# Performance work log

Measured on AMD Instinct MI355X. Metric: run time of the kernel, lower is better.

The kernel has to match this reference:

```python
import jax, jax.numpy as jnp
import numpy as np

P, N, M, B = 5, 30000, 50000, 256
T, C, L, ED, H, EMB, TD, NL = 13, 16, 3, 4, 128, 64, 5, 3
SRC = jnp.repeat(jnp.arange(P), P)  # edge type i = src*P + dst
DST = jnp.tile(jnp.arange(P), P)


def _affine(x, W, b):
    # x: [P, n, i], W: [P, i, o], b: [P, o]
    return jnp.einsum('pni,pio->pno', x, W) + b[:, None, :]


def _lrelu(x, s=0.01):
    return jnp.where(x >= 0, x, s * x)


def _gat(h, W, a_s, a_d, We, a_e, b, edge_index, edge_attr):
    # h: [P, N, H]; per-edge-type GATConv (heads=1, no self loops) then hetero 'max' aggregation
    hs, hd = h[SRC], h[DST]                       # [25, N, H]
    xl = jnp.einsum('enh,ehf->enf', hs, W)        # transformed source features
    xr = jnp.einsum('enh,ehf->enf', hd, W)
    als = jnp.einsum('enf,ef->en', xl, a_s)
    ald = jnp.einsum('enf,ef->en', xr, a_d)

    def per_type(xl_e, als_e, ald_e, ea, We_e, ae_e, ei):
        src, dst = ei[0], ei[1]
        alpha = als_e[src] + ald_e[dst] + (ea @ We_e) @ ae_e
        alpha = jnp.where(alpha >= 0, alpha, 0.2 * alpha)  # GAT negative_slope=0.2
        amax = jax.ops.segment_max(alpha, dst, num_segments=N)
        ex = jnp.exp(alpha - amax[dst])
        den = jax.ops.segment_sum(ex, dst, num_segments=N)
        w = ex / (den[dst] + 1e-16)
        return jax.ops.segment_sum(w[:, None] * xl_e[src], dst, num_segments=N)

    out = jax.vmap(per_type)(xl, als, ald, edge_attr, We, a_e, edge_index)
    out = out + b[:, None, :]
    return out.reshape(P, P, N, H).max(axis=0)  # HeteroConv aggr='max' over source types


def setup_inputs():
    key = jax.random.key(0)
    ks = iter(jax.random.split(key, 64))
    def nrm(shape, s=1.0):
        return jax.random.normal(next(ks), shape, dtype=jnp.float32) * s
    w = 0.05
    inp = {
        'x': nrm((P, N, T)),
        'cond_x': nrm((P, N, C + L)),
        'edge_attr': nrm((P * P, M, ED)),
        'timesteps': jax.random.uniform(next(ks), (B,), dtype=jnp.float32),
        'te1_W': nrm((1, TD), w), 'te1_b': nrm((TD,), w),
        'te2_W': nrm((TD, TD), w), 'te2_b': nrm((TD,), w),
        'emb_W': nrm((P, T + L, EMB), w), 'emb_b': nrm((P, EMB), w),
        'cemb_W': nrm((P, C, EMB), w), 'cemb_b': nrm((P, EMB), w),
        'pa_W': nrm((P, 2 * EMB, 2 * EMB), w), 'pa_b': nrm((P, 2 * EMB), w),
        'pc_W': nrm((P, 2 * EMB, EMB), w), 'pc_b': nrm((P, EMB), w),
        'sl0_W': nrm((P, EMB + TD, H), w), 'sl0_b': nrm((P, H), w),
        'sl12_W': nrm((2, P, H + TD, H), w), 'sl12_b': nrm((2, P, H), w),
        'slout_W': nrm((P, H + TD, T), w), 'slout_b': nrm((P, T), w),
        'gat_W': nrm((NL, P * P, H, H), w), 'gat_as': nrm((NL, P * P, H), w),
        'gat_ad': nrm((NL, P * P, H), w), 'gat_We': nrm((NL, P * P, ED, H), w),
        'gat_ae': nrm((NL, P * P, H), w), 'gat_b': nrm((NL, P * P, H), w),
        'xc_W': nrm((NL, P, H, H // 2), w), 'xc_b': nrm((NL, P, H // 2), w),
        'cc_W': nrm((NL, P, H, H // 2), w), 'cc_b': nrm((NL, P, H // 2), w),
        'ca_W': nrm((NL, P, H, H), w), 'ca_b': nrm((NL, P, H), w),
        'batch_idx': jax.random.randint(next(ks), (P, N), 0, B),
        'edge_index': jax.random.randint(next(ks), (P * P, 2, M), 0, N),
    }
    return inp


def reference(x, cond_x, edge_attr, timesteps, te1_W, te1_b, te2_W, te2_b,
              emb_W, emb_b, cemb_W, cemb_b, pa_W, pa_b, pc_W, pc_b,
              sl0_W, sl0_b, sl12_W, sl12_b, slout_W, slout_b,
              gat_W, gat_as, gat_ad, gat_We, gat_ae, gat_b,
              xc_W, xc_b, cc_W, cc_b, ca_W, ca_b, batch_idx, edge_index):
    # time embedding: Linear(1,TD) -> SiLU -> Linear(TD,TD)
    temb = jax.nn.silu(timesteps[:, None] @ te1_W + te1_b) @ te2_W + te2_b  # [B, TD]
    cond, latent = cond_x[..., :C], cond_x[..., C:]
    h = _affine(jnp.concatenate([x, latent], -1), emb_W, emb_b)            # [P,N,EMB]
    ce = _affine(cond, cemb_W, cemb_b)
    h = jnp.concatenate([h, ce], -1)                                       # [P,N,2EMB]
    h = jax.nn.sigmoid(_affine(h, pa_W, pa_b)) * h                         # attention pooling
    h = _affine(h, pc_W, pc_b)                                             # [P,N,EMB]
    nt = temb[batch_idx]                                                   # [P,N,TD]
    h = jnp.concatenate([h, nt], -1)
    for l in range(NL):
        if l > 0:
            h = jnp.concatenate([h, nt], -1)
        Wl, bl = (sl0_W, sl0_b) if l == 0 else (sl12_W[l - 1], sl12_b[l - 1])
        h = _lrelu(_affine(h, Wl, bl))                                     # [P,N,H]
        comm = _lrelu(_gat(h, gat_W[l], gat_as[l], gat_ad[l], gat_We[l], gat_ae[l], gat_b[l], edge_index, edge_attr))
        h = jnp.concatenate([_affine(h, xc_W[l], xc_b[l]), _affine(comm, cc_W[l], cc_b[l])], -1)
        h = h + jax.nn.sigmoid(_affine(h, ca_W[l], ca_b[l])) * h
    h = jnp.concatenate([h, nt], -1)
    return _affine(h, slout_W, slout_b)                                    # [P,N,T]
```

## Files before the change

kernel.cpp:

```cpp
#include <hip/hip_runtime.h>
#include <cstdio>

using bf8 = __attribute__((ext_vector_type(8))) short;
using f4v = __attribute__((ext_vector_type(4))) float;
typedef unsigned short u16;
typedef unsigned int u32;

#define DEV __device__ __forceinline__

DEV float bf2f(u16 u){ return __uint_as_float(((u32)u) << 16); }
DEV u16 f2bf(float f){ u32 u = __float_as_uint(f); return (u16)((u + 0x7fffu + ((u >> 16) & 1u)) >> 16); }
DEV float sigm(float v){ return 1.f / (1.f + __expf(-v)); }

constexpr int P5 = 5, NN = 30000, MM = 50000, NE = 25, BB = 256;
constexpr int KC = 96;
constexpr int RS = KC * 2 + 16;
constexpr int RSA = 272;

__global__ void temb_k(const float* ts, const float* w1, const float* b1,
                       const float* w2, const float* b2, float* temb){
  int i = blockIdx.x * blockDim.x + threadIdx.x;
  if (i >= BB) return;
  float t = ts[i]; float z[5];
#pragma unroll
  for (int j = 0; j < 5; ++j){ float u = t * w1[j] + b1[j]; z[j] = u * sigm(u); }
#pragma unroll
  for (int j2 = 0; j2 < 5; ++j2){
    float s = b2[j2];
#pragma unroll
    for (int j = 0; j < 5; ++j) s += z[j] * w2[j * 5 + j2];
    temb[i * 5 + j2] = s;
  }
}

__global__ void wtransE_k(const float* __restrict__ W, u16* __restrict__ Wt,
                          int Kreal, int Kpad, int Nreal, int Nalloc, int total){
  int idx = blockIdx.x * blockDim.x + threadIdx.x;
  if (idx >= total) return;
  int k = idx % Kpad;
  int t2 = idx / Kpad;
  int f = t2 % Nalloc;
  int b = t2 / Nalloc;
  float v = (k < Kreal && f < Nreal) ? W[((size_t)b * Kreal + k) * Nreal + f] : 0.f;
  Wt[idx] = f2bf(v);
}

__global__ void embw_k(const float* emb_W, const float* emb_b, const float* cemb_W, const float* cemb_b,
                       u16* Wc, float* bc){
  int b = blockIdx.x, f = threadIdx.x;
  for (int k = 0; k < 32; ++k){
    float v = 0.f;
    if (f < 64){ if (k < 16) v = emb_W[((size_t)b * 16 + k) * 64 + f]; }
    else       { if (k >= 16) v = cemb_W[((size_t)b * 16 + (k - 16)) * 64 + (f - 64)]; }
    Wc[((size_t)b * 128 + f) * 32 + k] = f2bf(v);
  }
  bc[b * 128 + f] = (f < 64) ? emb_b[b * 64 + f] : cemb_b[b * 64 + (f - 64)];
}

__global__ void gwtT_k(const float* __restrict__ gW, u16* __restrict__ gWt){
  int idx = blockIdx.x * blockDim.x + threadIdx.x;
  if (idx >= 75 * 128 * 128) return;
  int h = idx & 127, f = (idx >> 7) & 127, le = idx >> 14;
  gWt[idx] = f2bf(gW[(size_t)le * 16384 + h * 128 + f]);
}

__global__ void gatred_k(const float* gW, const float* gas, const float* gad,
                         const float* gWe, const float* gae,
                         float* wswd, float* eaw){
  int le = blockIdx.x; int h = threadIdx.x;
  const float* W = gW + (size_t)le * 16384;
  const float* as_ = gas + le * 128;
  const float* ad_ = gad + le * 128;
  float wsv = 0.f, wdv = 0.f;
  for (int f = 0; f < 128; ++f){
    float w = W[h * 128 + f];
    wsv += w * as_[f]; wdv += w * ad_[f];
  }
  wswd[le * 256 + h] = wsv;
  wswd[le * 256 + 128 + h] = wdv;
  if (h < 4){
    const float* We = gWe + (size_t)le * 512;
    const float* ae = gae + le * 128;
    float s = 0.f;
    for (int f = 0; f < 128; ++f) s += We[h * 128 + f] * ae[f];
    eaw[le * 4 + h] = s;
  }
}

__global__ void abuild_k(const float* x, const float* cx, u16* A0){
  int idx = blockIdx.x * blockDim.x + threadIdx.x;
  if (idx >= P5 * NN) return;
  const float* xr = x + (size_t)idx * 13;
  const float* cr = cx + (size_t)idx * 19;
  u16* a0 = A0 + (size_t)idx * 32;
#pragma unroll
  for (int i = 0; i < 13; ++i) a0[i] = f2bf(xr[i]);
#pragma unroll
  for (int i = 0; i < 3; ++i) a0[13 + i] = f2bf(cr[16 + i]);
#pragma unroll
  for (int i = 0; i < 16; ++i) a0[16 + i] = f2bf(cr[i]);
}

__global__ void ntfill_k(u16* buf, int pitch, int co, const int* bidx, const float* temb){
  int idx = blockIdx.x * blockDim.x + threadIdx.x;
  if (idx >= P5 * NN) return;
  int b = bidx[idx];
  u16* r = buf + (size_t)idx * pitch;
#pragma unroll
  for (int j = 0; j < 5; ++j) r[co + j] = f2bf(temb[b * 5 + j]);
  for (int j = co + 5; j < pitch; ++j) r[j] = 0;
}

__global__ void csr_count_k(const int* EI, int* cnt){
  int idx = blockIdx.x * blockDim.x + threadIdx.x;
  if (idx >= NE * MM) return;
  int e = idx / MM, m = idx % MM;
  int dst = EI[(size_t)e * 2 * MM + MM + m];
  atomicAdd(&cnt[e * NN + dst], 1);
}

__global__ __launch_bounds__(1024) void csr_scan_k(const int* cnt, int* off){
  int e = blockIdx.x, tid = threadIdx.x;
  int lane = tid & 63, wv = tid >> 6;
  __shared__ int wsum[16];
  int running = 0;
  for (int c = 0; c < 30; ++c){
    int idx = c * 1024 + tid;
    int v = (idx < NN) ? cnt[e * NN + idx] : 0;
    int s = v;
#pragma unroll
    for (int o = 1; o < 64; o <<= 1){
      int t = __shfl_up(s, o, 64);
      if (lane >= o) s += t;
    }
    if (lane == 63) wsum[wv] = s;
    __syncthreads();
    if (wv == 0 && lane < 16){
      int t = wsum[lane];
#pragma unroll
      for (int o = 1; o < 16; o <<= 1){
        int u = __shfl_up(t, o, 64);
        if (lane >= o) t += u;
      }
      wsum[lane] = t;
    }
    __syncthreads();
    int base = running + ((wv > 0) ? wsum[wv - 1] : 0);
    if (idx < NN) off[(size_t)e * (NN + 1) + idx] = base + s - v;
    running += wsum[15];
    __syncthreads();
  }
  if (tid == 0) off[(size_t)e * (NN + 1) + NN] = running;
}

__global__ void csr_fill_k(const int* EI, const int* off, int* cnt, int* mpos, int* srcC){
  int idx = blockIdx.x * blockDim.x + threadIdx.x;
  if (idx >= NE * MM) return;
  int e = idx / MM, m = idx % MM;
  int dst = EI[(size_t)e * 2 * MM + MM + m];
  int pos = off[(size_t)e * (NN + 1) + dst] + atomicAdd(&cnt[e * NN + dst], 1);
  mpos[idx] = pos;
  srcC[(size_t)e * MM + pos] = EI[(size_t)e * 2 * MM + m];
}

__global__ void eadot_k(const float* __restrict__ ea, const float* __restrict__ eaw,
                        const int* __restrict__ mpos, float* __restrict__ eadot){
  int idx = blockIdx.x * blockDim.x + threadIdx.x;
  if (idx >= 3 * NE * MM) return;
  int l = idx / (NE * MM);
  int rem = idx - l * NE * MM;
  int e = rem / MM, m = rem - e * MM;
  const float* a4 = ea + ((size_t)e * MM + m) * 4;
  const float* ew = eaw + (size_t)(l * NE + e) * 4;
  float d = a4[0] * ew[0] + a4[1] * ew[1] + a4[2] * ew[2] + a4[3] * ew[3];
  eadot[(size_t)l * NE * MM + (size_t)e * MM + mpos[rem]] = d;
}

__global__ __launch_bounds__(256) void dots2_k(const u16* __restrict__ hS, const float* __restrict__ wswd_l,
                                               float* __restrict__ als, float* __restrict__ ald){
  __shared__ u32 hl[64][65];
  __shared__ float wsl[10][129];
  int p = blockIdx.y;
  int n0 = blockIdx.x * 64;
  int tid = threadIdx.x;
  for (int i = tid; i < 10 * 128; i += 256){
    int col = i >> 7, k = i & 127;
    int e = (col < 5) ? (p * 5 + col) : ((col - 5) * 5 + p);
    wsl[col][k] = wswd_l[e * 256 + ((col < 5) ? 0 : 128) + k];
  }
  for (int i = tid; i < 64 * 64; i += 256){
    int r = i >> 6, kp = i & 63;
    int n = n0 + r;
    hl[r][kp] = (n < NN) ? ((const u32*)hS)[((size_t)p * NN + n) * 64 + kp] : 0u;
  }
  __syncthreads();
  int col = tid & 15, rbase = tid >> 4;
  if (col < 10){
#pragma unroll
    for (int pass = 0; pass < 4; ++pass){
      int r = rbase + pass * 16;
      int n = n0 + r;
      if (n >= NN) continue;
      float s = 0.f;
#pragma unroll
      for (int kp = 0; kp < 64; ++kp){
        u32 pr = hl[r][kp];
        s += bf2f((u16)(pr & 0xffffu)) * wsl[col][2 * kp]
           + bf2f((u16)(pr >> 16)) * wsl[col][2 * kp + 1];
      }
      if (col < 5) als[(size_t)(p * 5 + col) * NN + n] = s;
      else         ald[(size_t)((col - 5) * 5 + p) * NN + n] = s;
    }
  }
}

__global__ __launch_bounds__(256) void aexp_k(const float* __restrict__ als, const float* __restrict__ ald,
                                              const float* __restrict__ eadot_l, const int* __restrict__ srcC,
                                              const int* __restrict__ off, uint2* __restrict__ prec){
  int idx = blockIdx.x * blockDim.x + threadIdx.x;
  if (idx >= NE * NN) return;
  int e = idx / NN;
  int ro = off[(size_t)e + idx], re = off[(size_t)e + idx + 1];
  if (ro >= re) return;
  float av = ald[idx];
  const int* sc = srcC + (size_t)e * MM;
  const float* ed = eadot_l + (size_t)e * MM;
  const float* ale = als + (size_t)e * NN;
  float mx = -3.0e38f;
  for (int j = ro; j < re; ++j){
    float a = ale[sc[j]] + av + ed[j];
    a = (a >= 0.f) ? a : 0.2f * a;
    mx = fmaxf(mx, a);
  }
  for (int j = ro; j < re; ++j){
    int src = sc[j];
    float a = ale[src] + av + ed[j];
    a = (a >= 0.f) ? a : 0.2f * a;
    uint2 pr; pr.x = (u32)src; pr.y = __float_as_uint(__expf(a - mx));
    prec[(size_t)e * MM + j] = pr;
  }
}

__global__ __launch_bounds__(256) void agg3_k(const u16* __restrict__ hS, const uint2* __restrict__ prec,
                                              const int* __restrict__ off, u16* __restrict__ agghB,
                                              int pd0, int npd){
  int l = threadIdx.x & 63, w = threadIdx.x >> 6;
  int n0 = blockIdx.x * 8 + w;
  int n1 = n0 + 4;
  int y = blockIdx.y;
  int ps = y / npd, e = ps * 5 + pd0 + (y - ps * npd);
  const uint2* pe = prec + (size_t)e * MM;
  const int* offe = off + (size_t)e * (NN + 1);
  const u32* hb = (const u32*)hS + (size_t)ps * NN * 64 + l;
  int ro0 = 0, ln0 = 0, ro1 = 0, ln1 = 0;
  if (n0 < NN){ ro0 = offe[n0]; ln0 = offe[n0 + 1] - ro0; }
  if (n1 < NN){ ro1 = offe[n1]; ln1 = offe[n1 + 1] - ro1; }
  float den0 = 0.f, a00 = 0.f, a01 = 0.f;
  float den1 = 0.f, a10 = 0.f, a11 = 0.f;
  int mx = (ln0 > ln1) ? ln0 : ln1;
  for (int t = 0; t < mx; ++t){
    if (t < ln0){
      uint2 pr = pe[ro0 + t];
      float ex = __uint_as_float(pr.y);
      u32 hv = hb[(size_t)pr.x * 64];
      den0 += ex; a00 += ex * bf2f((u16)(hv & 0xffffu)); a01 += ex * bf2f((u16)(hv >> 16));
    }
    if (t < ln1){
      uint2 pr = pe[ro1 + t];
      float ex = __uint_as_float(pr.y);
      u32 hv = hb[(size_t)pr.x * 64];
      den1 += ex; a10 += ex * bf2f((u16)(hv & 0xffffu)); a11 += ex * bf2f((u16)(hv >> 16));
    }
  }
  if (n0 < NN){
    float inv = 1.f / (den0 + 1e-16f);
    ((u32*)agghB)[((size_t)y * NN + n0) * 64 + l] = (u32)f2bf(a00 * inv) | ((u32)f2bf(a01 * inv) << 16);
  }
  if (n1 < NN){
    float inv = 1.f / (den1 + 1e-16f);
    ((u32*)agghB)[((size_t)y * NN + n1) * 64 + l] = (u32)f2bf(a10 * inv) | ((u32)f2bf(a11 * inv) << 16);
  }
}

template<int NF, int MI, int NJ, int EPI, bool ALRELU>
__global__ __launch_bounds__(256) void tgemm_k(const u16* __restrict__ A, const u16* __restrict__ Wt,
                                               const float* __restrict__ bias, void* __restrict__ out,
                                               const u16* __restrict__ X,
                                               int Kpad, int opitch, int ocol, int xpitch){
  constexpr int Nalloc = NF * 16;
  constexpr int WR = 128 / (MI * 16);
  constexpr int WC = 4 / WR;
  static_assert(WR * WC == 4 && NJ * WC * 16 == Nalloc, "wave tiling");
  extern __shared__ __align__(16) char smem[];
  float* Cs = (float*)smem;
  const int tid = threadIdx.x;
  const int l = tid & 63, w = tid >> 6;
  const int bz = blockIdx.z;
  const int r0 = blockIdx.x * 128;
  const int wr = w / WC, wc = w % WC;
  const size_t Ab = (size_t)bz * NN;

  f4v acc[MI][NJ];
#pragma unroll
  for (int i = 0; i < MI; ++i)
#pragma unroll
    for (int j = 0; j < NJ; ++j) acc[i][j] = f4v{0.f, 0.f, 0.f, 0.f};

  for (int kb = 0; kb < Kpad; kb += KC){
    int kc = Kpad - kb; if (kc > KC) kc = KC;
    int nseg = kc >> 3;
    for (int s = tid; s < 128 * nseg; s += 256){
      int r = s / nseg, c = s - r * nseg;
      int grow = r0 + r; if (grow > NN - 1) grow = NN - 1;
      uint4 v = *(const uint4*)(A + (Ab + grow) * Kpad + kb + c * 8);
      if (ALRELU){
        u32 pr[4] = {v.x, v.y, v.z, v.w};
#pragma unroll
        for (int q = 0; q < 4; ++q){
          float lo = bf2f((u16)(pr[q] & 0xffffu)), hi = bf2f((u16)(pr[q] >> 16));
          lo = lo >= 0.f ? lo : 0.01f * lo; hi = hi >= 0.f ? hi : 0.01f * hi;
          pr[q] = (u32)f2bf(lo) | ((u32)f2bf(hi) << 16);
        }
        v.x = pr[0]; v.y = pr[1]; v.z = pr[2]; v.w = pr[3];
      }
      *(uint4*)(smem + r * RS + c * 16) = v;
    }
    for (int s = tid; s < Nalloc * nseg; s += 256){
      int r = s / nseg, c = s - r * nseg;
      uint4 v = *(const uint4*)(Wt + ((size_t)bz * Nalloc + r) * Kpad + kb + c * 8);
      *(uint4*)(smem + 128 * RS + r * RS + c * 16) = v;
    }
    __syncthreads();
    int KI = kc >> 5;
    for (int k0 = 0; k0 < KI; ++k0){
      bf8 af[MI], bfr[NJ];
#pragma unroll
      for (int i = 0; i < MI; ++i){
        int row = wr * (MI * 16) + i * 16 + (l & 15);
        af[i] = *(const bf8*)(smem + row * RS + k0 * 64 + (l >> 4) * 16);
      }
#pragma unroll
      for (int j = 0; j < NJ; ++j){
        int col = wc * (NJ * 16) + j * 16 + (l & 15);
        bfr[j] = *(const bf8*)(smem + 128 * RS + col * RS + k0 * 64 + (l >> 4) * 16);
      }
#pragma unroll
      for (int i = 0; i < MI; ++i)
#pragma unroll
        for (int j = 0; j < NJ; ++j)
          acc[i][j] = __builtin_amdgcn_mfma_f32_16x16x32_bf16(af[i], bfr[j], acc[i][j], 0, 0, 0);
    }
    __syncthreads();
  }

  if (EPI == 4){
    int col = l & 15;
    if (col < 13){
#pragma unroll
      for (int i = 0; i < MI; ++i){
        float bv = bias[bz * 13 + col];
#pragma unroll
        for (int r = 0; r < 4; ++r){
          int grow = r0 + wr * (MI * 16) + i * 16 + (l >> 4) * 4 + r;
          if (grow < NN)
            ((float*)out)[((size_t)bz * NN + grow) * 13 + col] = acc[i][0][r] + bv;
        }
      }
    }
    return;
  }

#pragma unroll
  for (int i = 0; i < MI; ++i)
#pragma unroll
    for (int j = 0; j < NJ; ++j){
      int tcol = wc * (NJ * 16) + j * 16 + (l & 15);
      float bv = bias[bz * Nalloc + tcol];
#pragma unroll
      for (int r = 0; r < 4; ++r){
        int trow = wr * (MI * 16) + i * 16 + (l >> 4) * 4 + r;
        float v = acc[i][j][r] + bv;
        if (EPI == 2) v = v >= 0.f ? v : 0.01f * v;
        Cs[trow * Nalloc + tcol] = v;
      }
    }
  __syncthreads();
  constexpr int nsc = Nalloc / 4;
  u16* o16 = (u16*)out;
  for (int s = tid; s < 128 * nsc; s += 256){
    int r = s / nsc, c = s - r * nsc;
    int grow = r0 + r; if (grow >= NN) continue;
    float4 cv = *(const float4*)(Cs + r * Nalloc + c * 4);
    float v0 = cv.x, v1 = cv.y, v2 = cv.z, v3 = cv.w;
    if (EPI == 1 || EPI == 3){
      uint2 xv = *(const uint2*)(X + ((size_t)bz * NN + grow) * xpitch + c * 4);
      float x0 = bf2f((u16)(xv.x & 0xffffu)), x1 = bf2f((u16)(xv.x >> 16));
      float x2 = bf2f((u16)(xv.y & 0xffffu)), x3 = bf2f((u16)(xv.y >> 16));
      if (EPI == 1){ v0 = x0 * sigm(v0); v1 = x1 * sigm(v1); v2 = x2 * sigm(v2); v3 = x3 * sigm(v3); }
      else { v0 = x0 * (1.f + sigm(v0)); v1 = x1 * (1.f + sigm(v1)); v2 = x2 * (1.f + sigm(v2)); v3 = x3 * (1.f + sigm(v3)); }
    }
    uint2 ov;
    ov.x = (u32)f2bf(v0) | ((u32)f2bf(v1) << 16);
    ov.y = (u32)f2bf(v2) | ((u32)f2bf(v3) << 16);
    *(uint2*)(o16 + ((size_t)bz * NN + grow) * opitch + ocol + c * 4) = ov;
  }
}

__global__ __launch_bounds__(256) void tgatmm_k(const u16* __restrict__ agghB, const u16* __restrict__ gWt_l,
                                                const float* __restrict__ gb_l, u16* __restrict__ comm,
                                                int pd){
  extern __shared__ __align__(16) char smem[];
  char* As = smem;
  char* Bs = smem + 128 * RSA;
  float* Cs = (float*)smem;
  const int tid = threadIdx.x, l = tid & 63, w = tid >> 6;
  const int r0 = blockIdx.x * 128;
  const int wr = w >> 1, wc = w & 1;
  f4v vmax[4][4];
#pragma unroll 1
  for (int ps = 0; ps < 5; ++ps){
    int e = ps * 5 + pd;
    const u16* aggs = agghB + (size_t)ps * NN * 128;
    const u16* wb = gWt_l + (size_t)e * 16384;
    for (int s = tid; s < 128 * 16; s += 256){
      int r = s >> 4, c = s & 15;
      int grow = r0 + r; if (grow > NN - 1) grow = NN - 1;
      *(uint4*)(As + r * RSA + c * 16) = *(const uint4*)(aggs + (size_t)grow * 128 + c * 8);
      *(uint4*)(Bs + r * RSA + c * 16) = *(const uint4*)(wb + r * 128 + c * 8);
    }
    __syncthreads();
    f4v acc[4][4];
#pragma unroll
    for (int i = 0; i < 4; ++i)
#pragma unroll
      for (int j = 0; j < 4; ++j) acc[i][j] = f4v{0.f, 0.f, 0.f, 0.f};
#pragma unroll
    for (int k0 = 0; k0 < 4; ++k0){
      bf8 af[4], bfr[4];
#pragma unroll
      for (int i = 0; i < 4; ++i)
        af[i] = *(const bf8*)(As + (wr * 64 + i * 16 + (l & 15)) * RSA + k0 * 64 + (l >> 4) * 16);
#pragma unroll
      for (int j = 0; j < 4; ++j)
        bfr[j] = *(const bf8*)(Bs + (wc * 64 + j * 16 + (l & 15)) * RSA + k0 * 64 + (l >> 4) * 16);
#pragma unroll
      for (int i = 0; i < 4; ++i)
#pragma unroll
        for (int j = 0; j < 4; ++j)
          acc[i][j] = __builtin_amdgcn_mfma_f32_16x16x32_bf16(af[i], bfr[j], acc[i][j], 0, 0, 0);
    }
    const float* be = gb_l + e * 128;
#pragma unroll
    for (int i = 0; i < 4; ++i)
#pragma unroll
      for (int j = 0; j < 4; ++j){
        int tcol = wc * 64 + j * 16 + (l & 15);
        float bv = be[tcol];
#pragma unroll
        for (int r = 0; r < 4; ++r){
          float cvv = acc[i][j][r] + bv;
          vmax[i][j][r] = (ps == 0) ? cvv : fmaxf(vmax[i][j][r], cvv);
        }
      }
    __syncthreads();
  }
#pragma unroll
  for (int i = 0; i < 4; ++i)
#pragma unroll
    for (int j = 0; j < 4; ++j){
      int tcol = wc * 64 + j * 16 + (l & 15);
#pragma unroll
      for (int r = 0; r < 4; ++r){
        int trow = wr * 64 + i * 16 + (l >> 4) * 4 + r;
        Cs[trow * 128 + tcol] = vmax[i][j][r];
      }
    }
  __syncthreads();
  for (int s = tid; s < 128 * 32; s += 256){
    int r = s >> 5, c = s & 31;
    int grow = r0 + r; if (grow >= NN) continue;
    float4 cv = *(const float4*)(Cs + r * 128 + c * 4);
    uint2 ov;
    ov.x = (u32)f2bf(cv.x) | ((u32)f2bf(cv.y) << 16);
    ov.y = (u32)f2bf(cv.z) | ((u32)f2bf(cv.w) << 16);
    *(uint2*)(comm + ((size_t)pd * NN + grow) * 128 + c * 4) = ov;
  }
}

constexpr size_t ALN(size_t x){ return (x + 255) & ~(size_t)255; }
constexpr size_t SZ_A0   = ALN((size_t)P5 * NN * 32 * 2);
constexpr size_t SZ_H0   = ALN((size_t)P5 * NN * 96 * 2);
constexpr size_t SZ_H128 = ALN((size_t)P5 * NN * 128 * 2);
constexpr size_t SZ_HL   = ALN((size_t)P5 * NN * 160 * 2);
constexpr size_t O_A0 = 0;
constexpr size_t O_H0 = O_A0 + SZ_A0;
constexpr size_t O_AGG = 0;
constexpr size_t O_HCAT = O_H0 + SZ_H0;
constexpr size_t O_HG = O_HCAT + SZ_H128;
constexpr size_t O_HS = O_HG + SZ_H128;
constexpr size_t O_HL = O_HS + SZ_H128;
constexpr size_t O_TEMB = O_HL + SZ_HL;
constexpr size_t O_WSWD = O_TEMB + ALN(256 * 5 * 4);
constexpr size_t O_EAW  = O_WSWD + ALN(75 * 256 * 4);
constexpr size_t O_CNT  = O_EAW + ALN(75 * 4 * 4);
constexpr size_t O_OFFS = O_CNT + ALN((size_t)NE * NN * 4);
constexpr size_t O_MPOS = O_OFFS + ALN((size_t)NE * (NN + 1) * 4);
constexpr size_t O_ALS  = O_MPOS + ALN((size_t)NE * MM * 4);
constexpr size_t O_ALD  = O_ALS + ALN((size_t)NE * NN * 4);
constexpr size_t O_SRCC = O_ALD + ALN((size_t)NE * NN * 4);
constexpr size_t O_EADOT= O_SRCC + ALN((size_t)NE * MM * 4);
constexpr size_t O_GWT  = O_EADOT + ALN((size_t)3 * NE * MM * 4);
constexpr size_t O_WCMB = O_GWT + ALN((size_t)75 * 16384 * 2);
constexpr size_t O_BCMB = O_WCMB + ALN((size_t)5 * 128 * 32 * 2);
constexpr size_t O_WPA  = O_BCMB + ALN((size_t)5 * 128 * 4);
constexpr size_t O_WPC  = O_WPA + ALN((size_t)5 * 128 * 128 * 2);
constexpr size_t O_WSL0 = O_WPC + ALN((size_t)5 * 64 * 128 * 2);
constexpr size_t O_WSL12= O_WSL0 + ALN((size_t)5 * 128 * 96 * 2);
constexpr size_t O_WSLO = O_WSL12 + ALN((size_t)10 * 128 * 160 * 2);
constexpr size_t O_WXC  = O_WSLO + ALN((size_t)5 * 16 * 160 * 2);
constexpr size_t O_WCC  = O_WXC + ALN((size_t)15 * 64 * 128 * 2);
constexpr size_t O_WCA  = O_WCC + ALN((size_t)15 * 64 * 128 * 2);
constexpr size_t O_PREC = O_WCA + ALN((size_t)15 * 128 * 128 * 2);
constexpr size_t WS_NEED= O_PREC + ALN((size_t)NE * MM * 8);

extern "C" void kernel_launch(void* const* d_in, const int* in_sizes, int n_in,
                              void* d_out, int out_size, void* d_ws, size_t ws_size,
                              hipStream_t stream){
  if (ws_size < WS_NEED){
    fprintf(stderr, "kernel_launch: ws too small: need %zu have %zu\n", WS_NEED, ws_size);
    return;
  }
  const float* x        = (const float*)d_in[0];
  const float* cond_x   = (const float*)d_in[1];
  const float* edge_attr= (const float*)d_in[2];
  const float* timesteps= (const float*)d_in[3];
  const float* te1_W = (const float*)d_in[4];
  const float* te1_b = (const float*)d_in[5];
  const float* te2_W = (const float*)d_in[6];
  const float* te2_b = (const float*)d_in[7];
  const float* emb_W = (const float*)d_in[8];
  const float* emb_b = (const float*)d_in[9];
  const float* cemb_W= (const float*)d_in[10];
  const float* cemb_b= (const float*)d_in[11];
  const float* pa_W  = (const float*)d_in[12];
  const float* pa_b  = (const float*)d_in[13];
  const float* pc_W  = (const float*)d_in[14];
  const float* pc_b  = (const float*)d_in[15];
  const float* sl0_W = (const float*)d_in[16];
  const float* sl0_b = (const float*)d_in[17];
  const float* sl12_W= (const float*)d_in[18];
  const float* sl12_b= (const float*)d_in[19];
  const float* slout_W=(const float*)d_in[20];
  const float* slout_b=(const float*)d_in[21];
  const float* gat_W = (const float*)d_in[22];
  const float* gat_as= (const float*)d_in[23];
  const float* gat_ad= (const float*)d_in[24];
  const float* gat_We= (const float*)d_in[25];
  const float* gat_ae= (const float*)d_in[26];
  const float* gat_b = (const float*)d_in[27];
  const float* xc_W  = (const float*)d_in[28];
  const float* xc_b  = (const float*)d_in[29];
  const float* cc_W  = (const float*)d_in[30];
  const float* cc_b  = (const float*)d_in[31];
  const float* ca_W  = (const float*)d_in[32];
  const float* ca_b  = (const float*)d_in[33];
  const int* batch_idx = (const int*)d_in[34];
  const int* edge_index= (const int*)d_in[35];

  char* ws = (char*)d_ws;
  u16* A0    = (u16*)(ws + O_A0);
  u16* h0buf = (u16*)(ws + O_H0);
  u16* agghB = (u16*)(ws + O_AGG);
  u16* hcat  = (u16*)(ws + O_HCAT);
  u16* hg    = (u16*)(ws + O_HG);
  u16* h2    = (u16*)(ws + O_HG);
  u16* hS    = (u16*)(ws + O_HS);
  u16* hL    = (u16*)(ws + O_HL);
  u16* comm  = (u16*)(ws + O_HL);
  float* tembp = (float*)(ws + O_TEMB);
  float* wswdp = (float*)(ws + O_WSWD);
  float* eawp  = (float*)(ws + O_EAW);
  int* cnt  = (int*)(ws + O_CNT);
  int* offs = (int*)(ws + O_OFFS);
  int* mposp= (int*)(ws + O_MPOS);
  float* alsp = (float*)(ws + O_ALS);
  float* aldp = (float*)(ws + O_ALD);
  int* srcCp = (int*)(ws + O_SRCC);
  float* eadotp = (float*)(ws + O_EADOT);
  u16* gwt   = (u16*)(ws + O_GWT);
  u16* wcmb  = (u16*)(ws + O_WCMB);
  float* bcmb= (float*)(ws + O_BCMB);
  u16* wpa   = (u16*)(ws + O_WPA);
  u16* wpc   = (u16*)(ws + O_WPC);
  u16* wsl0  = (u16*)(ws + O_WSL0);
  u16* wsl12 = (u16*)(ws + O_WSL12);
  u16* wslo  = (u16*)(ws + O_WSLO);
  u16* wxc   = (u16*)(ws + O_WXC);
  u16* wcc   = (u16*)(ws + O_WCC);
  u16* wca   = (u16*)(ws + O_WCA);
  uint2* precp = (uint2*)(ws + O_PREC);

  const dim3 B256(256);
  const dim3 TG(235, 1, 5);
  const int GPN = (P5 * NN + 255) / 256;
  const int GEM = (NE * MM + 255) / 256;
  const int GEN = (NE * NN + 255) / 256;
  constexpr int LDS_N128 = 65536;
  constexpr int LDS_N64  = 39936;
  constexpr int LDS_SLO  = 29952;
  constexpr int LDS_TGAT = 128 * RSA * 2;

  temb_k<<<1, B256, 0, stream>>>(timesteps, te1_W, te1_b, te2_W, te2_b, tembp);
  embw_k<<<5, 128, 0, stream>>>(emb_W, emb_b, cemb_W, cemb_b, wcmb, bcmb);
  {
    auto WT = [&](const float* W, u16* Wt, int Kr, int Kp, int Nr, int Na, int B){
      int total = B * Na * Kp;
      wtransE_k<<<(total + 255) / 256, B256, 0, stream>>>(W, Wt, Kr, Kp, Nr, Na, total);
    };
    WT(pa_W, wpa, 128, 128, 128, 128, 5);
    WT(pc_W, wpc, 128, 128, 64, 64, 5);
    WT(sl0_W, wsl0, 69, 96, 128, 128, 5);
    WT(sl12_W, wsl12, 133, 160, 128, 128, 10);
    WT(slout_W, wslo, 133, 160, 13, 16, 5);
    WT(xc_W, wxc, 128, 128, 64, 64, 15);
    WT(cc_W, wcc, 128, 128, 64, 64, 15);
    WT(ca_W, wca, 128, 128, 128, 128, 15);
  }
  gwtT_k<<<(75 * 128 * 128 + 255) / 256, B256, 0, stream>>>(gat_W, gwt);
  gatred_k<<<75, 128, 0, stream>>>(gat_W, gat_as, gat_ad, gat_We, gat_ae, wswdp, eawp);

  hipMemsetAsync(cnt, 0, (size_t)NE * NN * 4, stream);
  csr_count_k<<<GEM, B256, 0, stream>>>(edge_index, cnt);
  csr_scan_k<<<25, 1024, 0, stream>>>(cnt, offs);
  hipMemsetAsync(cnt, 0, (size_t)NE * NN * 4, stream);
  csr_fill_k<<<GEM, B256, 0, stream>>>(edge_index, offs, cnt, mposp, srcCp);
  eadot_k<<<(3 * NE * MM + 255) / 256, B256, 0, stream>>>(edge_attr, eawp, mposp, eadotp);

  abuild_k<<<GPN, B256, 0, stream>>>(x, cond_x, A0);
  tgemm_k<8, 4, 4, 0, false><<<TG, B256, LDS_N128, stream>>>(A0, wcmb, bcmb, hcat, nullptr, 32, 128, 0, 0);
  tgemm_k<8, 4, 4, 1, false><<<TG, B256, LDS_N128, stream>>>(hcat, wpa, pa_b, hg, hcat, 128, 128, 0, 128);
  tgemm_k<4, 2, 4, 0, false><<<TG, B256, LDS_N64, stream>>>(hg, wpc, pc_b, h0buf, nullptr, 128, 96, 0, 0);
  ntfill_k<<<GPN, B256, 0, stream>>>(h0buf, 96, 64, batch_idx, tembp);

  for (int l = 0; l < 3; ++l){
    if (l == 0)
      tgemm_k<8, 4, 4, 2, false><<<TG, B256, LDS_N128, stream>>>(h0buf, wsl0, sl0_b, hS, nullptr, 96, 128, 0, 0);
    else
      tgemm_k<8, 4, 4, 2, false><<<TG, B256, LDS_N128, stream>>>(hL, wsl12 + (size_t)(l - 1) * 5 * 128 * 160,
                                                                 sl12_b + (size_t)(l - 1) * 5 * 128, hS, nullptr,
                                                                 160, 128, 0, 0);
    const float* wswd_l = wswdp + (size_t)l * 25 * 256;
    const u16* gwt_l = gwt + (size_t)l * 25 * 16384;
    const float* gb_l = gat_b + (size_t)l * 25 * 128;
    dots2_k<<<dim3(469, 5), B256, 0, stream>>>(hS, wswd_l, alsp, aldp);
    aexp_k<<<GEN, B256, 0, stream>>>(alsp, aldp, eadotp + (size_t)l * NE * MM, srcCp, offs, precp);
    for (int pd = 0; pd < 5; ++pd){
      agg3_k<<<dim3(3750, 5), B256, 0, stream>>>(hS, precp, offs, agghB, pd, 1);
      tgatmm_k<<<dim3(235), B256, LDS_TGAT, stream>>>(agghB, gwt_l, gb_l, comm, pd);
    }
    tgemm_k<4, 2, 4, 0, false><<<TG, B256, LDS_N64, stream>>>(hS, wxc + (size_t)l * 5 * 64 * 128,
                                                              xc_b + (size_t)l * 5 * 64, h2, nullptr,
                                                              128, 128, 0, 0);
    tgemm_k<4, 2, 4, 0, true><<<TG, B256, LDS_N64, stream>>>(comm, wcc + (size_t)l * 5 * 64 * 128,
                                                             cc_b + (size_t)l * 5 * 64, h2, nullptr,
                                                             128, 128, 64, 0);
    tgemm_k<8, 4, 4, 3, false><<<TG, B256, LDS_N128, stream>>>(h2, wca + (size_t)l * 5 * 128 * 128,
                                                               ca_b + (size_t)l * 5 * 128, hL, h2,
                                                               128, 160, 0, 128);
    ntfill_k<<<GPN, B256, 0, stream>>>(hL, 160, 128, batch_idx, tembp);
  }

  tgemm_k<1, 2, 1, 4, false><<<TG, B256, LDS_SLO, stream>>>(hL, wslo, slout_b, d_out, nullptr, 160, 13, 0, 0);
}
```

Before: 1.956 ms.

## Fuse per-layer xc/cc/ca GEMMs into one kernel and build CSR in LDS

Replaces the three per-layer GEMM launches (xc, cc, ca) with a single 512-thread kernel. It computes both 64-wide halves, keeps the concatenated h2 tile in LDS, and applies the gated residual before writing hL, which removes the h2 round trip through global memory. Separately, the CSR count, scan and fill steps become one kernel per edge type that uses LDS atomics, dropping two memsets, two launches and the global count buffer. In exchange, the CSR build runs on only 25 blocks, so parallelism there is low, and the order of edges within a destination bucket becomes nondeterministic.

```diff
diff --git a/kernel.cpp b/kernel.cpp
--- a/kernel.cpp
+++ b/kernel.cpp
@@ -111,56 +111,48 @@
   for (int j = co + 5; j < pitch; ++j) r[j] = 0;
 }
 
-__global__ void csr_count_k(const int* EI, int* cnt){
-  int idx = blockIdx.x * blockDim.x + threadIdx.x;
-  if (idx >= NE * MM) return;
-  int e = idx / MM, m = idx % MM;
-  int dst = EI[(size_t)e * 2 * MM + MM + m];
-  atomicAdd(&cnt[e * NN + dst], 1);
-}
-
-__global__ __launch_bounds__(1024) void csr_scan_k(const int* cnt, int* off){
+__global__ __launch_bounds__(1024) void csr_build_k(const int* __restrict__ EI, int* __restrict__ off,
+                                                    int* __restrict__ mpos, int* __restrict__ srcC){
+  extern __shared__ int cntl[];
+  __shared__ int wsum[16];
   int e = blockIdx.x, tid = threadIdx.x;
   int lane = tid & 63, wv = tid >> 6;
-  __shared__ int wsum[16];
+  for (int i = tid; i < NN; i += 1024) cntl[i] = 0;
+  __syncthreads();
+  const int* srcp = EI + (size_t)e * 2 * MM;
+  const int* dstp = srcp + MM;
+  for (int m = tid; m < MM; m += 1024) atomicAdd(&cntl[dstp[m]], 1);
+  __syncthreads();
   int running = 0;
   for (int c = 0; c < 30; ++c){
     int idx = c * 1024 + tid;
-    int v = (idx < NN) ? cnt[e * NN + idx] : 0;
+    int v = (idx < NN) ? cntl[idx] : 0;
     int s = v;
 #pragma unroll
-    for (int o = 1; o < 64; o <<= 1){
-      int t = __shfl_up(s, o, 64);
-      if (lane >= o) s += t;
-    }
+    for (int o = 1; o < 64; o <<= 1){ int t = __shfl_up(s, o, 64); if (lane >= o) s += t; }
     if (lane == 63) wsum[wv] = s;
     __syncthreads();
     if (wv == 0 && lane < 16){
       int t = wsum[lane];
 #pragma unroll
-      for (int o = 1; o < 16; o <<= 1){
-        int u = __shfl_up(t, o, 64);
-        if (lane >= o) t += u;
-      }
+      for (int o = 1; o < 16; o <<= 1){ int u = __shfl_up(t, o, 64); if (lane >= o) t += u; }
       wsum[lane] = t;
     }
     __syncthreads();
     int base = running + ((wv > 0) ? wsum[wv - 1] : 0);
-    if (idx < NN) off[(size_t)e * (NN + 1) + idx] = base + s - v;
+    int ex = base + s - v;
+    if (idx < NN){ off[(size_t)e * (NN + 1) + idx] = ex; cntl[idx] = ex; }
     running += wsum[15];
     __syncthreads();
   }
   if (tid == 0) off[(size_t)e * (NN + 1) + NN] = running;
-}
-
-__global__ void csr_fill_k(const int* EI, const int* off, int* cnt, int* mpos, int* srcC){
-  int idx = blockIdx.x * blockDim.x + threadIdx.x;
-  if (idx >= NE * MM) return;
-  int e = idx / MM, m = idx % MM;
-  int dst = EI[(size_t)e * 2 * MM + MM + m];
-  int pos = off[(size_t)e * (NN + 1) + dst] + atomicAdd(&cnt[e * NN + dst], 1);
-  mpos[idx] = pos;
-  srcC[(size_t)e * MM + pos] = EI[(size_t)e * 2 * MM + m];
+  __syncthreads();
+  for (int m = tid; m < MM; m += 1024){
+    int d = dstp[m];
+    int pos = atomicAdd(&cntl[d], 1);
+    mpos[(size_t)e * MM + m] = pos;
+    srcC[(size_t)e * MM + pos] = srcp[m];
+  }
 }
 
 __global__ void eadot_k(const float* __restrict__ ea, const float* __restrict__ eaw,
@@ -392,12 +384,11 @@
     int grow = r0 + r; if (grow >= NN) continue;
     float4 cv = *(const float4*)(Cs + r * Nalloc + c * 4);
     float v0 = cv.x, v1 = cv.y, v2 = cv.z, v3 = cv.w;
-    if (EPI == 1 || EPI == 3){
+    if (EPI == 1){
       uint2 xv = *(const uint2*)(X + ((size_t)bz * NN + grow) * xpitch + c * 4);
       float x0 = bf2f((u16)(xv.x & 0xffffu)), x1 = bf2f((u16)(xv.x >> 16));
       float x2 = bf2f((u16)(xv.y & 0xffffu)), x3 = bf2f((u16)(xv.y >> 16));
-      if (EPI == 1){ v0 = x0 * sigm(v0); v1 = x1 * sigm(v1); v2 = x2 * sigm(v2); v3 = x3 * sigm(v3); }
-      else { v0 = x0 * (1.f + sigm(v0)); v1 = x1 * (1.f + sigm(v1)); v2 = x2 * (1.f + sigm(v2)); v3 = x3 * (1.f + sigm(v3)); }
+      v0 = x0 * sigm(v0); v1 = x1 * sigm(v1); v2 = x2 * sigm(v2); v3 = x3 * sigm(v3);
     }
     uint2 ov;
     ov.x = (u32)f2bf(v0) | ((u32)f2bf(v1) << 16);
@@ -487,6 +478,164 @@
   }
 }
 
+__global__ __launch_bounds__(512) void fca_k(const u16* __restrict__ hS, const u16* __restrict__ comm,
+                                             const u16* __restrict__ wxc_l, const float* __restrict__ bxc_l,
+                                             const u16* __restrict__ wcc_l, const float* __restrict__ bcc_l,
+                                             const u16* __restrict__ wca_l, const float* __restrict__ bca_l,
+                                             u16* __restrict__ hL){
+  extern __shared__ __align__(16) char smem[];
+  char* As = smem;
+  char* H2 = smem + 128 * RSA;
+  const int tid = threadIdx.x, l = tid & 63, wv = tid >> 6;
+  const int wr = wv >> 1, wc = wv & 1;
+  const int bz = blockIdx.z;
+  const int r0 = blockIdx.x * 128;
+  const size_t pb = (size_t)bz * NN;
+
+  f4v acc_a[2][2], acc_b[2][2];
+  for (int s = tid; s < 128 * 16; s += 512){
+    int r = s >> 4, c = s & 15;
+    int grow = r0 + r; if (grow > NN - 1) grow = NN - 1;
+    *(uint4*)(As + r * RSA + c * 16) = *(const uint4*)(hS + (pb + grow) * 128 + c * 8);
+  }
+  for (int s = tid; s < 64 * 16; s += 512){
+    int r = s >> 4, c = s & 15;
+    *(uint4*)(H2 + r * RSA + c * 16) = *(const uint4*)(wxc_l + (size_t)bz * 8192 + r * 128 + c * 8);
+  }
+  __syncthreads();
+#pragma unroll
+  for (int i = 0; i < 2; ++i)
+#pragma unroll
+    for (int j = 0; j < 2; ++j) acc_a[i][j] = f4v{0.f, 0.f, 0.f, 0.f};
+#pragma unroll
+  for (int k0 = 0; k0 < 4; ++k0){
+    bf8 af[2], bfr[2];
+#pragma unroll
+    for (int i = 0; i < 2; ++i)
+      af[i] = *(const bf8*)(As + (wr * 32 + i * 16 + (l & 15)) * RSA + k0 * 64 + (l >> 4) * 16);
+#pragma unroll
+    for (int j = 0; j < 2; ++j)
+      bfr[j] = *(const bf8*)(H2 + (wc * 32 + j * 16 + (l & 15)) * RSA + k0 * 64 + (l >> 4) * 16);
+#pragma unroll
+    for (int i = 0; i < 2; ++i)
+#pragma unroll
+      for (int j = 0; j < 2; ++j)
+        acc_a[i][j] = __builtin_amdgcn_mfma_f32_16x16x32_bf16(af[i], bfr[j], acc_a[i][j], 0, 0, 0);
+  }
+  __syncthreads();
+  for (int s = tid; s < 128 * 16; s += 512){
+    int r = s >> 4, c = s & 15;
+    int grow = r0 + r; if (grow > NN - 1) grow = NN - 1;
+    uint4 v = *(const uint4*)(comm + (pb + grow) * 128 + c * 8);
+    u32 pr[4] = {v.x, v.y, v.z, v.w};
+#pragma unroll
+    for (int q = 0; q < 4; ++q){
+      float lo = bf2f((u16)(pr[q] & 0xffffu)), hi = bf2f((u16)(pr[q] >> 16));
+      lo = lo >= 0.f ? lo : 0.01f * lo; hi = hi >= 0.f ? hi : 0.01f * hi;
+      pr[q] = (u32)f2bf(lo) | ((u32)f2bf(hi) << 16);
+    }
+    v.x = pr[0]; v.y = pr[1]; v.z = pr[2]; v.w = pr[3];
+    *(uint4*)(As + r * RSA + c * 16) = v;
+  }
+  for (int s = tid; s < 64 * 16; s += 512){
+    int r = s >> 4, c = s & 15;
+    *(uint4*)(H2 + r * RSA + c * 16) = *(const uint4*)(wcc_l + (size_t)bz * 8192 + r * 128 + c * 8);
+  }
+  __syncthreads();
+#pragma unroll
+  for (int i = 0; i < 2; ++i)
+#pragma unroll
+    for (int j = 0; j < 2; ++j) acc_b[i][j] = f4v{0.f, 0.f, 0.f, 0.f};
+#pragma unroll
+  for (int k0 = 0; k0 < 4; ++k0){
+    bf8 af[2], bfr[2];
+#pragma unroll
+    for (int i = 0; i < 2; ++i)
+      af[i] = *(const bf8*)(As + (wr * 32 + i * 16 + (l & 15)) * RSA + k0 * 64 + (l >> 4) * 16);
+#pragma unroll
+    for (int j = 0; j < 2; ++j)
+      bfr[j] = *(const bf8*)(H2 + (wc * 32 + j * 16 + (l & 15)) * RSA + k0 * 64 + (l >> 4) * 16);
+#pragma unroll
+    for (int i = 0; i < 2; ++i)
+#pragma unroll
+      for (int j = 0; j < 2; ++j)
+        acc_b[i][j] = __builtin_amdgcn_mfma_f32_16x16x32_bf16(af[i], bfr[j], acc_b[i][j], 0, 0, 0);
+  }
+  __syncthreads();
+#pragma unroll
+  for (int i = 0; i < 2; ++i)
+#pragma unroll
+    for (int j = 0; j < 2; ++j){
+      int colL = wc * 32 + j * 16 + (l & 15);
+      float bL = bxc_l[bz * 64 + colL];
+      float bR = bcc_l[bz * 64 + colL];
+#pragma unroll
+      for (int r = 0; r < 4; ++r){
+        int row = wr * 32 + i * 16 + (l >> 4) * 4 + r;
+        *(u16*)(H2 + row * RSA + colL * 2)       = f2bf(acc_a[i][j][r] + bL);
+        *(u16*)(H2 + row * RSA + (colL + 64) * 2) = f2bf(acc_b[i][j][r] + bR);
+      }
+    }
+  for (int s = tid; s < 128 * 16; s += 512){
+    int r = s >> 4, c = s & 15;
+    *(uint4*)(As + r * RSA + c * 16) = *(const uint4*)(wca_l + (size_t)bz * 16384 + r * 128 + c * 8);
+  }
+  __syncthreads();
+  f4v acc_g[2][4];
+#pragma unroll
+  for (int i = 0; i < 2; ++i)
+#pragma unroll
+    for (int j = 0; j < 4; ++j) acc_g[i][j] = f4v{0.f, 0.f, 0.f, 0.f};
+#pragma unroll
+  for (int k0 = 0; k0 < 4; ++k0){
+    bf8 af[2], bfr[4];
+#pragma unroll
+    for (int i = 0; i < 2; ++i)
+      af[i] = *(const bf8*)(H2 + (wr * 32 + i * 16 + (l & 15)) * RSA + k0 * 64 + (l >> 4) * 16);
+#pragma unroll
+    for (int j = 0; j < 4; ++j)
+      bfr[j] = *(const bf8*)(As + (wc * 64 + j * 16 + (l & 15)) * RSA + k0 * 64 + (l >> 4) * 16);
+#pragma unroll
+    for (int i = 0; i < 2; ++i)
+#pragma unroll
+      for (int j = 0; j < 4; ++j)
+        acc_g[i][j] = __builtin_amdgcn_mfma_f32_16x16x32_bf16(af[i], bfr[j], acc_g[i][j], 0, 0, 0);
+  }
+  float vout[2][4][4];
+#pragma unroll
+  for (int i = 0; i < 2; ++i)
+#pragma unroll
+    for (int j = 0; j < 4; ++j){
+      int col = wc * 64 + j * 16 + (l & 15);
+      float bv = bca_l[bz * 128 + col];
+#pragma unroll
+      for (int r = 0; r < 4; ++r){
+        int row = wr * 32 + i * 16 + (l >> 4) * 4 + r;
+        float xg = bf2f(*(const u16*)(H2 + row * RSA + col * 2));
+        vout[i][j][r] = xg * (1.f + sigm(acc_g[i][j][r] + bv));
+      }
+    }
+  __syncthreads();
+#pragma unroll
+  for (int i = 0; i < 2; ++i)
+#pragma unroll
+    for (int j = 0; j < 4; ++j){
+      int col = wc * 64 + j * 16 + (l & 15);
+#pragma unroll
+      for (int r = 0; r < 4; ++r){
+        int row = wr * 32 + i * 16 + (l >> 4) * 4 + r;
+        *(u16*)(H2 + row * RSA + col * 2) = f2bf(vout[i][j][r]);
+      }
+    }
+  __syncthreads();
+  for (int s = tid; s < 128 * 32; s += 512){
+    int r = s >> 5, c = s & 31;
+    int grow = r0 + r; if (grow >= NN) continue;
+    uint2 v = *(const uint2*)(H2 + r * RSA + c * 8);
+    *(uint2*)(hL + (pb + grow) * 160 + c * 4) = v;
+  }
+}
+
 constexpr size_t ALN(size_t x){ return (x + 255) & ~(size_t)255; }
 constexpr size_t SZ_A0   = ALN((size_t)P5 * NN * 32 * 2);
 constexpr size_t SZ_H0   = ALN((size_t)P5 * NN * 96 * 2);
@@ -502,8 +651,7 @@
 constexpr size_t O_TEMB = O_HL + SZ_HL;
 constexpr size_t O_WSWD = O_TEMB + ALN(256 * 5 * 4);
 constexpr size_t O_EAW  = O_WSWD + ALN(75 * 256 * 4);
-constexpr size_t O_CNT  = O_EAW + ALN(75 * 4 * 4);
-constexpr size_t O_OFFS = O_CNT + ALN((size_t)NE * NN * 4);
+constexpr size_t O_OFFS = O_EAW + ALN(75 * 4 * 4);
 constexpr size_t O_MPOS = O_OFFS + ALN((size_t)NE * (NN + 1) * 4);
 constexpr size_t O_ALS  = O_MPOS + ALN((size_t)NE * MM * 4);
 constexpr size_t O_ALD  = O_ALS + ALN((size_t)NE * NN * 4);
@@ -573,14 +721,12 @@
   u16* agghB = (u16*)(ws + O_AGG);
   u16* hcat  = (u16*)(ws + O_HCAT);
   u16* hg    = (u16*)(ws + O_HG);
-  u16* h2    = (u16*)(ws + O_HG);
+  u16* comm  = (u16*)(ws + O_HG);
   u16* hS    = (u16*)(ws + O_HS);
   u16* hL    = (u16*)(ws + O_HL);
-  u16* comm  = (u16*)(ws + O_HL);
   float* tembp = (float*)(ws + O_TEMB);
   float* wswdp = (float*)(ws + O_WSWD);
   float* eawp  = (float*)(ws + O_EAW);
-  int* cnt  = (int*)(ws + O_CNT);
   int* offs = (int*)(ws + O_OFFS);
   int* mposp= (int*)(ws + O_MPOS);
   float* alsp = (float*)(ws + O_ALS);
@@ -603,12 +749,13 @@
   const dim3 B256(256);
   const dim3 TG(235, 1, 5);
   const int GPN = (P5 * NN + 255) / 256;
-  const int GEM = (NE * MM + 255) / 256;
   const int GEN = (NE * NN + 255) / 256;
   constexpr int LDS_N128 = 65536;
   constexpr int LDS_N64  = 39936;
   constexpr int LDS_SLO  = 29952;
   constexpr int LDS_TGAT = 128 * RSA * 2;
+  constexpr int LDS_FCA  = 128 * RSA * 2;
+  constexpr int LDS_CSR  = NN * 4;
 
   temb_k<<<1, B256, 0, stream>>>(timesteps, te1_W, te1_b, te2_W, te2_b, tembp);
   embw_k<<<5, 128, 0, stream>>>(emb_W, emb_b, cemb_W, cemb_b, wcmb, bcmb);
@@ -629,11 +776,7 @@
   gwtT_k<<<(75 * 128 * 128 + 255) / 256, B256, 0, stream>>>(gat_W, gwt);
   gatred_k<<<75, 128, 0, stream>>>(gat_W, gat_as, gat_ad, gat_We, gat_ae, wswdp, eawp);
 
-  hipMemsetAsync(cnt, 0, (size_t)NE * NN * 4, stream);
-  csr_count_k<<<GEM, B256, 0, stream>>>(edge_index, cnt);
-  csr_scan_k<<<25, 1024, 0, stream>>>(cnt, offs);
-  hipMemsetAsync(cnt, 0, (size_t)NE * NN * 4, stream);
-  csr_fill_k<<<GEM, B256, 0, stream>>>(edge_index, offs, cnt, mposp, srcCp);
+  csr_build_k<<<25, 1024, LDS_CSR, stream>>>(edge_index, offs, mposp, srcCp);
   eadot_k<<<(3 * NE * MM + 255) / 256, B256, 0, stream>>>(edge_attr, eawp, mposp, eadotp);
 
   abuild_k<<<GPN, B256, 0, stream>>>(x, cond_x, A0);
@@ -658,15 +801,10 @@
       agg3_k<<<dim3(3750, 5), B256, 0, stream>>>(hS, precp, offs, agghB, pd, 1);
       tgatmm_k<<<dim3(235), B256, LDS_TGAT, stream>>>(agghB, gwt_l, gb_l, comm, pd);
     }
-    tgemm_k<4, 2, 4, 0, false><<<TG, B256, LDS_N64, stream>>>(hS, wxc + (size_t)l * 5 * 64 * 128,
-                                                              xc_b + (size_t)l * 5 * 64, h2, nullptr,
-                                                              128, 128, 0, 0);
-    tgemm_k<4, 2, 4, 0, true><<<TG, B256, LDS_N64, stream>>>(comm, wcc + (size_t)l * 5 * 64 * 128,
-                                                             cc_b + (size_t)l * 5 * 64, h2, nullptr,
-                                                             128, 128, 64, 0);
-    tgemm_k<8, 4, 4, 3, false><<<TG, B256, LDS_N128, stream>>>(h2, wca + (size_t)l * 5 * 128 * 128,
-                                                               ca_b + (size_t)l * 5 * 128, hL, h2,
-                                                               128, 160, 0, 128);
+    fca_k<<<dim3(235, 1, 5), 512, LDS_FCA, stream>>>(hS, comm,
+        wxc + (size_t)l * 5 * 64 * 128, xc_b + (size_t)l * 5 * 64,
+        wcc + (size_t)l * 5 * 64 * 128, cc_b + (size_t)l * 5 * 64,
+        wca + (size_t)l * 5 * 128 * 128, ca_b + (size_t)l * 5 * 128, hL);
     ntfill_k<<<GPN, B256, 0, stream>>>(hL, 160, 128, batch_idx, tembp);
   }
 
```

Result: faster. 1.821 ms (-6.9%).
